# Kernel tuning notes

Hardware: AMD Instinct MI355X
Metric: run time of the kernel (lower is better)

Reference implementation:

```python
import jax, jax.numpy as jnp
import numpy as np

N, E = 20000, 320000
IN, HID, R, HEADS = 128, 256, 4, 4
C = HID // HEADS  # per-head dim


def setup_inputs() -> dict:
    key = jax.random.key(0)
    ks = jax.random.split(key, 20)
    g = lambda k, s, sc=0.05: jax.random.normal(k, s, jnp.float32) * sc
    return {
        'x': g(ks[0], (N, IN), 1.0),
        'edge_index': jax.random.randint(ks[1], (2, E), 0, N),
        'edge_type': jax.random.randint(ks[2], (E,), 0, R),
        'h_prev': g(ks[3], (N, HID), 1.0),
        # RGCN layer 1: relation weights, root weight, bias
        'W1': g(ks[4], (R, IN, HID)), 'root1': g(ks[5], (IN, HID)), 'b1': jnp.zeros((HID,), jnp.float32),
        # RGCN layer 2
        'W2': g(ks[6], (R, HID, HID)), 'root2': g(ks[7], (HID, HID)), 'b2': jnp.zeros((HID,), jnp.float32),
        # TransformerConv linears (query/key/value/skip), each Linear(HID, HEADS*C)
        'Wq': g(ks[8], (HID, HID)), 'bq': jnp.zeros((HID,), jnp.float32),
        'Wk': g(ks[9], (HID, HID)), 'bk': jnp.zeros((HID,), jnp.float32),
        'Wv': g(ks[10], (HID, HID)), 'bv': jnp.zeros((HID,), jnp.float32),
        'Wskip': g(ks[11], (HID, HID)), 'bskip': jnp.zeros((HID,), jnp.float32),
        # GRUCell (torch layout: [3*HID, in], gates ordered r, z, n)
        'W_ih': g(ks[12], (3 * HID, HID)), 'b_ih': jnp.zeros((3 * HID,), jnp.float32),
        'W_hh': g(ks[13], (3 * HID, HID)), 'b_hh': jnp.zeros((3 * HID,), jnp.float32),
    }


def rgcn(x, src, dst, etype, W, Wroot, b):
    # PyG RGCNConv: out_i = x_i @ Wroot + b + sum_r mean_{j in N_r(i)} x_j @ W_r
    n = x.shape[0]
    out = x @ Wroot + b
    xs = x[src]  # [E, F_in]
    for r in range(W.shape[0]):  # small fixed relation count
        mask = (etype == r).astype(x.dtype)  # [E]
        msg = (xs @ W[r]) * mask[:, None]  # [E, F_out]
        agg = jax.ops.segment_sum(msg, dst, num_segments=n)
        cnt = jax.ops.segment_sum(mask, dst, num_segments=n)
        out = out + agg / jnp.maximum(cnt, 1.0)[:, None]
    return out


def transformer_conv(x, src, dst, Wq, bq, Wk, bk, Wv, bv, Wskip, bskip):
    # PyG TransformerConv, concat=True, root_weight=True
    n = x.shape[0]
    q = (x @ Wq + bq).reshape(n, HEADS, C)
    k = (x @ Wk + bk).reshape(n, HEADS, C)
    v = (x @ Wv + bv).reshape(n, HEADS, C)
    score = jnp.einsum('ehc,ehc->eh', q[dst], k[src]) * (1.0 / np.sqrt(C))  # [E, H]
    smax = jax.ops.segment_max(score, dst, num_segments=n)  # [N, H]
    ex = jnp.exp(score - smax[dst])
    denom = jax.ops.segment_sum(ex, dst, num_segments=n)
    alpha = ex / jnp.maximum(denom[dst], 1e-16)  # edge softmax per dst node
    out = jax.ops.segment_sum(alpha[:, :, None] * v[src], dst, num_segments=n)  # [N, H, C]
    return out.reshape(n, HEADS * C) + x @ Wskip + bskip


def gru_cell(xi, h, W_ih, b_ih, W_hh, b_hh):
    gi = xi @ W_ih.T + b_ih
    gh = h @ W_hh.T + b_hh
    ir, iz, inn = jnp.split(gi, 3, axis=1)
    hr, hz, hn = jnp.split(gh, 3, axis=1)
    r = jax.nn.sigmoid(ir + hr)
    z = jax.nn.sigmoid(iz + hz)
    nw = jnp.tanh(inn + r * hn)
    return (1.0 - z) * nw + z * h


def reference(x, edge_index, edge_type, h_prev, W1, root1, b1, W2, root2, b2,
              Wq, bq, Wk, bk, Wv, bv, Wskip, bskip, W_ih, b_ih, W_hh, b_hh):
    src, dst = edge_index[0], edge_index[1]
    h = jax.nn.relu(rgcn(x, src, dst, edge_type, W1, root1, b1))
    h = jax.nn.relu(rgcn(h, src, dst, edge_type, W2, root2, b2))
    h = transformer_conv(h, src, dst, Wq, bq, Wk, bk, Wv, bv, Wskip, bskip)
    h = gru_cell(h, h_prev, W_ih, b_ih, W_hh, b_hh)
    return h
```

## Files before the change

kernel.cpp:

```cpp
#include <hip/hip_runtime.h>
#include <hip/hip_bf16.h>
#include <stdint.h>

#define N_NODES 20000
#define E_EDGES 320000
#define IN_F    128
#define HIDF    256
#define R_REL   4
#define NRKEYS  (N_NODES*R_REL)
#define SCAN_BLOCKS 80

typedef __attribute__((ext_vector_type(8))) short  short8;
typedef __attribute__((ext_vector_type(4))) float  floatx4;

__device__ __forceinline__ float bf2f(__hip_bfloat16 v){ return __bfloat162float(v); }
__device__ __forceinline__ __hip_bfloat16 f2bf(float v){ return __float2bfloat16(v); }
__device__ __forceinline__ float bfbits2f(unsigned short u){ return __uint_as_float(((unsigned)u)<<16); }
__device__ __forceinline__ unsigned short f2bfbits(float v){
    __hip_bfloat16 h = __float2bfloat16(v);
    return *(unsigned short*)&h;
}
__device__ __forceinline__ unsigned pack_bf2(float a, float b){
    return (unsigned)f2bfbits(a) | ((unsigned)f2bfbits(b) << 16);
}

__device__ __forceinline__ void gload_lds16(const void* g, void* l)
{
    __builtin_amdgcn_global_load_lds((const __attribute__((address_space(1))) void*)g,
                                     (__attribute__((address_space(3))) void*)l, 16, 0, 0);
}

template<int N>
__device__ __forceinline__ void wait_vm()
{
    if constexpr (N == 0)      asm volatile("s_waitcnt vmcnt(0)" ::: "memory");
    else if constexpr (N == 3) asm volatile("s_waitcnt vmcnt(3)" ::: "memory");
    else if constexpr (N == 4) asm volatile("s_waitcnt vmcnt(4)" ::: "memory");
    else if constexpr (N == 5) asm volatile("s_waitcnt vmcnt(5)" ::: "memory");
    else if constexpr (N == 8) asm volatile("s_waitcnt vmcnt(8)" ::: "memory");
    else                       asm volatile("s_waitcnt vmcnt(0)" ::: "memory");
}

__device__ __forceinline__ int2 xcd_swizzle()
{
    int gx = gridDim.x, gy = gridDim.y;
    int nwg = gx * gy;
    int lin = blockIdx.x + gx * blockIdx.y;
    int q = nwg >> 3, r = nwg & 7;
    int k = lin & 7, i = lin >> 3;
    int j = (k < r ? k*(q+1) : r*(q+1) + (k-r)*q) + i;
    return make_int2(j / gy, j % gy);
}

__global__ void count_kernel(const int* __restrict__ ei, const int* __restrict__ et,
                             int* __restrict__ cnt)
{
    int e = blockIdx.x*256 + threadIdx.x;
    if (e >= E_EDGES) return;
    int dst = ei[E_EDGES + e];
    atomicAdd(&cnt[dst*R_REL + et[e]], 1);
}

__global__ __launch_bounds__(1024) void scan_reduce_kernel(const int* __restrict__ cnt,
                                                           int* __restrict__ blocksum)
{
    int ix = blockIdx.x*1024 + threadIdx.x;
    int v = (ix < NRKEYS) ? cnt[ix] : 0;
    #pragma unroll
    for (int o=32;o>0;o>>=1) v += __shfl_xor(v, o, 64);
    __shared__ int wsum[16];
    int wave = threadIdx.x >> 6, lane = threadIdx.x & 63;
    if (lane == 0) wsum[wave] = v;
    __syncthreads();
    if (threadIdx.x == 0) {
        int s = 0;
        #pragma unroll
        for (int w=0;w<16;w++) s += wsum[w];
        blocksum[blockIdx.x] = s;
    }
}

__global__ __launch_bounds__(128) void scan_sums_kernel(const int* __restrict__ blocksum,
                                                        int* __restrict__ blockoff)
{
    __shared__ int s[128];
    int t = threadIdx.x;
    int v = (t < SCAN_BLOCKS) ? blocksum[t] : 0;
    s[t] = v; __syncthreads();
    for (int off=1; off<128; off<<=1) {
        int u = (t>=off) ? s[t-off] : 0;
        __syncthreads();
        s[t] += u;
        __syncthreads();
    }
    if (t < SCAN_BLOCKS) blockoff[t] = s[t] - v;
}

__global__ __launch_bounds__(1024) void scan_apply_kernel(const int* __restrict__ cnt,
                                                          const int* __restrict__ blockoff,
                                                          int* __restrict__ row_ptr,
                                                          int* __restrict__ cursor)
{
    __shared__ int s[1024];
    int t = threadIdx.x;
    int ix = blockIdx.x*1024 + t;
    int v = (ix < NRKEYS) ? cnt[ix] : 0;
    s[t] = v; __syncthreads();
    for (int off=1; off<1024; off<<=1) {
        int u = (t>=off) ? s[t-off] : 0;
        __syncthreads();
        s[t] += u;
        __syncthreads();
    }
    if (ix < NRKEYS) {
        int excl = blockoff[blockIdx.x] + s[t] - v;
        row_ptr[ix] = excl;
        cursor[ix]  = excl;
        if (ix == NRKEYS-1) row_ptr[NRKEYS] = excl + v;
    }
}

__global__ void fill_kernel(const int* __restrict__ ei, const int* __restrict__ et,
                            int* __restrict__ cursor, int* __restrict__ csr_src)
{
    int e = blockIdx.x*256 + threadIdx.x;
    if (e >= E_EDGES) return;
    int src = ei[e];
    int dst = ei[E_EDGES + e];
    int key = dst*R_REL + et[e];
    int pos = atomicAdd(&cursor[key], 1);
    csr_src[pos] = src;
}

__global__ void make_b1t(const float* __restrict__ root1,
                         const float* __restrict__ W1,
                         __hip_bfloat16* __restrict__ B1t)
{
    int idx = blockIdx.x*256 + threadIdx.x;
    if (idx >= 256*640) return;
    int n = idx / 640, k = idx % 640;
    float v;
    if (k < 128) v = root1[k*256 + n];
    else         v = W1[(k-128)*256 + n];
    B1t[idx] = f2bf(v);
}

__global__ void make_b2t(const float* __restrict__ root2,
                         const float* __restrict__ W2,
                         __hip_bfloat16* __restrict__ B2t)
{
    int idx = blockIdx.x*256 + threadIdx.x;
    if (idx >= 256*1280) return;
    int n = idx / 1280, k = idx % 1280;
    float v;
    if (k < 256) v = root2[k*256 + n];
    else         v = W2[(k-256)*256 + n];
    B2t[idx] = f2bf(v);
}

__global__ void make_b3t(const float* __restrict__ Wq, const float* __restrict__ Wk,
                         const float* __restrict__ Wv, const float* __restrict__ Wsk,
                         const float* __restrict__ bq, const float* __restrict__ bk,
                         const float* __restrict__ bv, const float* __restrict__ bsk,
                         __hip_bfloat16* __restrict__ B3t, float* __restrict__ bias3)
{
    int idx = blockIdx.x*256 + threadIdx.x;
    if (idx >= 1024*256) return;
    int n = idx / 256, k = idx % 256;
    int g = n >> 8, nn = n & 255;
    const float* W = (g==0)?Wq:(g==1)?Wk:(g==2)?Wv:Wsk;
    B3t[idx] = f2bf(W[k*256 + nn]);
    if (k == 0) {
        const float* B = (g==0)?bq:(g==1)?bk:(g==2)?bv:bsk;
        bias3[n] = B[nn];
    }
}

__global__ void cvt_f32_bf16(const float* __restrict__ in, __hip_bfloat16* __restrict__ out, int n)
{
    int i = blockIdx.x*256 + threadIdx.x;
    if (i < n) out[i] = f2bf(in[i]);
}

__global__ __launch_bounds__(256) void agg1_kernel(const float* __restrict__ x,
                                                   const int* __restrict__ row_ptr,
                                                   const int* __restrict__ csr_src,
                                                   __hip_bfloat16* __restrict__ A1)
{
    int b = blockIdx.x*4 + (threadIdx.x >> 6);
    int lane = threadIdx.x & 63;
    int i = b >> 2, r = b & 3;
    int e0 = row_ptr[b], e1 = row_ptr[b+1];
    float sx0=0.f,sy0=0.f, sx1=0.f,sy1=0.f, sx2=0.f,sy2=0.f, sx3=0.f,sy3=0.f;
    int e = e0;
    for (; e+4 <= e1; e += 4) {
        int i0=csr_src[e], i1=csr_src[e+1], i2=csr_src[e+2], i3=csr_src[e+3];
        float2 v0 = *(const float2*)(x + (size_t)i0*IN_F + lane*2);
        float2 v1 = *(const float2*)(x + (size_t)i1*IN_F + lane*2);
        float2 v2 = *(const float2*)(x + (size_t)i2*IN_F + lane*2);
        float2 v3 = *(const float2*)(x + (size_t)i3*IN_F + lane*2);
        sx0+=v0.x; sy0+=v0.y; sx1+=v1.x; sy1+=v1.y;
        sx2+=v2.x; sy2+=v2.y; sx3+=v3.x; sy3+=v3.y;
    }
    for (; e < e1; e++) {
        int i0 = csr_src[e];
        float2 v = *(const float2*)(x + (size_t)i0*IN_F + lane*2);
        sx0+=v.x; sy0+=v.y;
    }
    float sx = (sx0+sx1)+(sx2+sx3);
    float sy = (sy0+sy1)+(sy2+sy3);
    float inv = (e1>e0) ? 1.f/(float)(e1-e0) : 0.f;
    *(unsigned*)(A1 + (size_t)i*640 + 128 + r*128 + lane*2) = pack_bf2(sx*inv, sy*inv);
    if (r == 0) {
        float2 v = *(const float2*)(x + (size_t)i*IN_F + lane*2);
        *(unsigned*)(A1 + (size_t)i*640 + lane*2) = pack_bf2(v.x, v.y);
    }
}

__global__ __launch_bounds__(256) void agg2_kernel(const int* __restrict__ row_ptr,
                                                   const int* __restrict__ csr_src,
                                                   __hip_bfloat16* __restrict__ A2)
{
    int b = blockIdx.x*4 + (threadIdx.x >> 6);
    int lane = threadIdx.x & 63;
    int i = b >> 2, r = b & 3;
    int e0 = row_ptr[b], e1 = row_ptr[b+1];
    float a0=0.f,a1=0.f,a2=0.f,a3=0.f;
    float b0=0.f,b1=0.f,b2=0.f,b3=0.f;
    float c0=0.f,c1=0.f,c2=0.f,c3=0.f;
    float d0=0.f,d1=0.f,d2=0.f,d3=0.f;
    int e = e0;
    for (; e+4 <= e1; e += 4) {
        int i0=csr_src[e], i1=csr_src[e+1], i2=csr_src[e+2], i3=csr_src[e+3];
        ushort4 u0 = *(const ushort4*)(A2 + (size_t)i0*1280 + lane*4);
        ushort4 u1 = *(const ushort4*)(A2 + (size_t)i1*1280 + lane*4);
        ushort4 u2 = *(const ushort4*)(A2 + (size_t)i2*1280 + lane*4);
        ushort4 u3 = *(const ushort4*)(A2 + (size_t)i3*1280 + lane*4);
        a0+=bfbits2f(u0.x); a1+=bfbits2f(u0.y); a2+=bfbits2f(u0.z); a3+=bfbits2f(u0.w);
        b0+=bfbits2f(u1.x); b1+=bfbits2f(u1.y); b2+=bfbits2f(u1.z); b3+=bfbits2f(u1.w);
        c0+=bfbits2f(u2.x); c1+=bfbits2f(u2.y); c2+=bfbits2f(u2.z); c3+=bfbits2f(u2.w);
        d0+=bfbits2f(u3.x); d1+=bfbits2f(u3.y); d2+=bfbits2f(u3.z); d3+=bfbits2f(u3.w);
    }
    for (; e < e1; e++) {
        int i0 = csr_src[e];
        ushort4 u = *(const ushort4*)(A2 + (size_t)i0*1280 + lane*4);
        a0+=bfbits2f(u.x); a1+=bfbits2f(u.y); a2+=bfbits2f(u.z); a3+=bfbits2f(u.w);
    }
    float s0=(a0+b0)+(c0+d0), s1=(a1+b1)+(c1+d1), s2=(a2+b2)+(c2+d2), s3=(a3+b3)+(c3+d3);
    float inv = (e1>e0) ? 1.f/(float)(e1-e0) : 0.f;
    uint2 w;
    w.x = pack_bf2(s0*inv, s1*inv);
    w.y = pack_bf2(s2*inv, s3*inv);
    *(uint2*)(A2 + (size_t)i*1280 + 256 + r*256 + lane*4) = w;
}

template<int MI>
__device__ __forceinline__ void gemm_bt_body(const __hip_bfloat16* __restrict__ A, int lda,
                                             const __hip_bfloat16* __restrict__ Bt,
                                             const float* __restrict__ bias,
                                             __hip_bfloat16* __restrict__ C, int ldc,
                                             int M, int K, int relu,
                                             int tile_m, int tile_n,
                                             __hip_bfloat16* lds_a, __hip_bfloat16* lds_b)
{
    constexpr int A_ELEMS = MI*1024;
    constexpr int B_ELEMS = 4096;
    constexpr int L = MI/2 + 2;
    const int tid  = threadIdx.x;
    const int wave = tid >> 6;
    const int lane = tid & 63;
    const int wm = wave >> 1, wn = wave & 1;
    const int fm = lane & 15;
    const int q  = lane >> 4;
    const int sw = (q ^ ((fm >> 1) & 3)) * 8;

    floatx4 acc[MI][4];
    #pragma unroll
    for (int i=0;i<MI;i++)
        #pragma unroll
        for (int j=0;j<4;j++) acc[i][j] = (floatx4){0.f,0.f,0.f,0.f};

    const int srow   = lane >> 2;
    const int schunk = lane & 3;
    size_t a_goff[MI/2];
    #pragma unroll
    for (int s = 0; s < MI/2; ++s) {
        int r = (s*4 + wave)*16 + srow;
        int c = schunk ^ ((r >> 1) & 3);
        a_goff[s] = (size_t)min(tile_m + r, M-1)*lda + c*8;
    }
    size_t b_goff[2];
    #pragma unroll
    for (int s = 0; s < 2; ++s) {
        int r = (s*4 + wave)*16 + srow;
        int c = schunk ^ ((r >> 1) & 3);
        b_goff[s] = (size_t)(tile_n + r)*K + c*8;
    }

    const int nt = K >> 5;

    auto issue = [&](int t, int bufi) {
        const int kn = t << 5;
        #pragma unroll
        for (int s = 0; s < MI/2; ++s)
            gload_lds16(A + a_goff[s] + kn, lds_a + bufi*A_ELEMS + (s*4 + wave)*512);
        #pragma unroll
        for (int s = 0; s < 2; ++s)
            gload_lds16(Bt + b_goff[s] + kn, lds_b + bufi*B_ELEMS + (s*4 + wave)*512);
    };

    issue(0, 0);
    if (nt > 1) { issue(1, 1); wait_vm<L>(); }
    else        { wait_vm<0>(); }
    __builtin_amdgcn_s_barrier();

    int cur = 0, nx2 = 2;
    for (int t = 0; t < nt; ++t) {
        if (t + 2 < nt) issue(t + 2, nx2);

        const __hip_bfloat16* la = lds_a + cur*A_ELEMS;
        const __hip_bfloat16* lb = lds_b + cur*B_ELEMS;
        short8 afr[MI], bfr[4];
        #pragma unroll
        for (int i=0;i<MI;i++)
            afr[i] = *(const short8*)(la + (wm*(MI*16) + i*16 + fm)*32 + sw);
        #pragma unroll
        for (int j=0;j<4;j++)
            bfr[j] = *(const short8*)(lb + (wn*64 + j*16 + fm)*32 + sw);

        __builtin_amdgcn_s_setprio(1);
        #pragma unroll
        for (int i=0;i<MI;i++)
            #pragma unroll
            for (int j=0;j<4;j++)
                acc[i][j] = __builtin_amdgcn_mfma_f32_16x16x32_bf16(afr[i], bfr[j], acc[i][j], 0,0,0);
        __builtin_amdgcn_s_setprio(0);

        if (t + 1 < nt) {
            if (t + 2 < nt) wait_vm<L>();
            else            wait_vm<0>();
            __builtin_amdgcn_s_barrier();
            cur = (cur == 2) ? 0 : cur + 1;
            nx2 = (nx2 == 2) ? 0 : nx2 + 1;
        }
    }

    const int crow_base = tile_m + wm*(MI*16);
    const int ccol_base = tile_n + wn*64;
    #pragma unroll
    for (int i=0;i<MI;i++) {
        #pragma unroll
        for (int j=0;j<4;j++) {
            int c  = ccol_base + j*16 + fm;
            float bb = bias[c];
            #pragma unroll
            for (int rg=0; rg<4; rg++) {
                int r = crow_base + i*16 + q*4 + rg;
                if (r < M) {
                    float v = acc[i][j][rg] + bb;
                    if (relu) v = fmaxf(v, 0.f);
                    C[(size_t)r*ldc + c] = f2bf(v);
                }
            }
        }
    }
}

template<int MI>
__global__ __launch_bounds__(256) void gemm_bt_t(const __hip_bfloat16* __restrict__ A, int lda,
                                                 const __hip_bfloat16* __restrict__ Bt,
                                                 const float* __restrict__ bias,
                                                 __hip_bfloat16* __restrict__ C, int ldc,
                                                 int M, int K, int relu)
{
    __shared__ __align__(16) __hip_bfloat16 lds_a[3*MI*1024];
    __shared__ __align__(16) __hip_bfloat16 lds_b[3*4096];
    int2 xy = xcd_swizzle();
    gemm_bt_body<MI>(A, lda, Bt, bias, C, ldc, M, K, relu,
                     xy.x*(MI*32), xy.y*128, lds_a, lds_b);
}

__global__ __launch_bounds__(256) void gemm_gru_fused(
    const __hip_bfloat16* __restrict__ A0,
    const __hip_bfloat16* __restrict__ A1,
    const __hip_bfloat16* __restrict__ Bt0,
    const __hip_bfloat16* __restrict__ Bt1,
    const float* __restrict__ b_ih, const float* __restrict__ b_hh,
    const float* __restrict__ hprev, float* __restrict__ out)
{
    constexpr int BUF_ELEMS = 16384;
    __shared__ __align__(16) __hip_bfloat16 lds[2*BUF_ELEMS];
    int2 xy = xcd_swizzle();
    const int tile_m = xy.x * 64;
    const int c0     = xy.y * 64;
    const int tid = threadIdx.x, wave = tid >> 6, lane = tid & 63;
    const int wm = wave >> 1, wn = wave & 1;
    const int fm = lane & 15, q = lane >> 4;
    const int sw = (q ^ ((fm >> 1) & 3)) * 8;

    const int sub = lane >> 2, ch = lane & 3;
    const __hip_bfloat16* gsrc[8];
    int dstoff[8];
    #pragma unroll
    for (int s = 0; s < 8; ++s) {
        int seg = wave*8 + s;
        if (seg < 8) {
            int fr = seg*16 + sub;
            int mat = fr >> 6, rl = fr & 63;
            int c = ch ^ ((fr >> 1) & 3);
            int grow = min(tile_m + rl, N_NODES-1);
            gsrc[s] = (mat ? A1 : A0) + (size_t)grow*256 + c*8;
            dstoff[s] = seg*512;
        } else {
            int fs = seg - 8;
            int fr = fs*16 + sub;
            int grp = fr >> 6, ri = fr & 63;
            int mat = grp >= 3, gate = mat ? grp-3 : grp;
            int c = ch ^ ((fr >> 1) & 3);
            int grow = gate*256 + c0 + ri;
            gsrc[s] = (mat ? Bt1 : Bt0) + (size_t)grow*256 + c*8;
            dstoff[s] = 4096 + fs*512;
        }
    }

    floatx4 acc[2][3][2][2];
    #pragma unroll
    for (int m=0;m<2;m++)
        #pragma unroll
        for (int g=0;g<3;g++)
            #pragma unroll
            for (int i=0;i<2;i++)
                #pragma unroll
                for (int f=0;f<2;f++) acc[m][g][i][f] = (floatx4){0.f,0.f,0.f,0.f};

    auto issue = [&](int t, int bufi) {
        const int kn = t << 5;
        #pragma unroll
        for (int s = 0; s < 8; ++s)
            gload_lds16(gsrc[s] + kn, lds + bufi*BUF_ELEMS + dstoff[s]);
    };

    issue(0, 0);
    issue(1, 1);
    wait_vm<8>();
    __builtin_amdgcn_s_barrier();

    #pragma unroll 1
    for (int t = 0; t < 8; ++t) {
        const __hip_bfloat16* lb = lds + (t & 1)*BUF_ELEMS;
        short8 af[2][2], bfr[2][3][2];
        #pragma unroll
        for (int m=0;m<2;m++)
            #pragma unroll
            for (int i=0;i<2;i++)
                af[m][i] = *(const short8*)(lb + (m*64 + wm*32 + i*16 + fm)*32 + sw);
        #pragma unroll
        for (int m=0;m<2;m++)
            #pragma unroll
            for (int g=0;g<3;g++)
                #pragma unroll
                for (int f=0;f<2;f++)
                    bfr[m][g][f] = *(const short8*)(lb + 4096 + (((m*3+g)*64 + wn*32 + f*16 + fm)*32) + sw);

        __builtin_amdgcn_s_setprio(1);
        #pragma unroll
        for (int m=0;m<2;m++)
            #pragma unroll
            for (int g=0;g<3;g++)
                #pragma unroll
                for (int i=0;i<2;i++)
                    #pragma unroll
                    for (int f=0;f<2;f++)
                        acc[m][g][i][f] = __builtin_amdgcn_mfma_f32_16x16x32_bf16(af[m][i], bfr[m][g][f], acc[m][g][i][f], 0,0,0);
        __builtin_amdgcn_s_setprio(0);

        if (t + 1 < 8) {
            __builtin_amdgcn_s_barrier();
            if (t + 2 < 8) { issue(t + 2, t & 1); wait_vm<8>(); }
            else           wait_vm<0>();
            __builtin_amdgcn_s_barrier();
        }
    }

    #pragma unroll
    for (int f=0; f<2; ++f) {
        int c = c0 + wn*32 + f*16 + fm;
        float bir = b_ih[c], biz = b_ih[256+c], bin = b_ih[512+c];
        float bhr = b_hh[c], bhz = b_hh[256+c], bhn = b_hh[512+c];
        #pragma unroll
        for (int i=0; i<2; ++i) {
            #pragma unroll
            for (int rg=0; rg<4; ++rg) {
                int r = tile_m + wm*32 + i*16 + q*4 + rg;
                if (r < N_NODES) {
                    float gir = acc[0][0][i][f][rg] + bir;
                    float giz = acc[0][1][i][f][rg] + biz;
                    float gin = acc[0][2][i][f][rg] + bin;
                    float ghr = acc[1][0][i][f][rg] + bhr;
                    float ghz = acc[1][1][i][f][rg] + bhz;
                    float ghn = acc[1][2][i][f][rg] + bhn;
                    float rr = 1.f/(1.f + __expf(-(gir + ghr)));
                    float zz = 1.f/(1.f + __expf(-(giz + ghz)));
                    float xn = gin + rr*ghn;
                    float e2 = __expf(xn + xn);
                    float nn = 1.f - 2.f/(e2 + 1.f);
                    float h  = hprev[(size_t)r*256 + c];
                    out[(size_t)r*256 + c] = (1.f - zz)*nn + zz*h;
                }
            }
        }
    }
}

__global__ __launch_bounds__(256) void score_kernel(const __hip_bfloat16* __restrict__ qkvs,
                                                    const int* __restrict__ row_ptr,
                                                    const int* __restrict__ csr_src,
                                                    float* __restrict__ score)
{
    int i = blockIdx.x*4 + (threadIdx.x >> 6);
    int lane = threadIdx.x & 63;
    int h = lane >> 4, d4 = lane & 15;
    int e0 = row_ptr[i*R_REL], e1 = row_ptr[i*R_REL + R_REL];
    ushort4 qv = *(const ushort4*)(qkvs + (size_t)i*1024 + lane*4);
    float qx=bfbits2f(qv.x), qy=bfbits2f(qv.y), qz=bfbits2f(qv.z), qw=bfbits2f(qv.w);
    float* sp = score + (size_t)h*E_EDGES;
    int j = e0;
    for (; j+2 <= e1; j += 2) {
        int s0 = csr_src[j], s1 = csr_src[j+1];
        ushort4 k0 = *(const ushort4*)(qkvs + (size_t)s0*1024 + 256 + lane*4);
        ushort4 k1 = *(const ushort4*)(qkvs + (size_t)s1*1024 + 256 + lane*4);
        float d0 = qx*bfbits2f(k0.x)+qy*bfbits2f(k0.y)+qz*bfbits2f(k0.z)+qw*bfbits2f(k0.w);
        float d1 = qx*bfbits2f(k1.x)+qy*bfbits2f(k1.y)+qz*bfbits2f(k1.z)+qw*bfbits2f(k1.w);
        #pragma unroll
        for (int o=1;o<16;o<<=1){ d0 += __shfl_xor(d0,o,64); d1 += __shfl_xor(d1,o,64); }
        if (d4 == 0) { sp[j] = d0*0.125f; sp[j+1] = d1*0.125f; }
    }
    for (; j < e1; j++) {
        int s0 = csr_src[j];
        ushort4 k0 = *(const ushort4*)(qkvs + (size_t)s0*1024 + 256 + lane*4);
        float d0 = qx*bfbits2f(k0.x)+qy*bfbits2f(k0.y)+qz*bfbits2f(k0.z)+qw*bfbits2f(k0.w);
        #pragma unroll
        for (int o=1;o<16;o<<=1) d0 += __shfl_xor(d0,o,64);
        if (d4 == 0) sp[j] = d0*0.125f;
    }
}

__global__ __launch_bounds__(256) void attn_agg_kernel(const __hip_bfloat16* __restrict__ qkvs,
                                                       const float* __restrict__ score,
                                                       const int* __restrict__ row_ptr,
                                                       const int* __restrict__ csr_src,
                                                       __hip_bfloat16* __restrict__ hatt)
{
    int i = blockIdx.x*4 + (threadIdx.x >> 6);
    int lane = threadIdx.x & 63;
    int h  = lane >> 4;
    int d4 = lane & 15;
    int e0 = row_ptr[i*R_REL], e1 = row_ptr[i*R_REL + R_REL];
    int deg = e1 - e0;
    const float* sp = score + (size_t)h*E_EDGES + e0;

    float m = -1e30f;
    for (int j = d4; j < deg; j += 16) m = fmaxf(m, sp[j]);
    #pragma unroll
    for (int o=1;o<16;o<<=1) m = fmaxf(m, __shfl_xor(m, o, 64));

    float ssum = 0.f;
    for (int j = d4; j < deg; j += 16) ssum += __expf(sp[j] - m);
    #pragma unroll
    for (int o=1;o<16;o<<=1) ssum += __shfl_xor(ssum, o, 64);
    float inv = 1.f / fmaxf(ssum, 1e-16f);

    float ax=0.f, ay=0.f, az=0.f, aw=0.f;
    int j = 0;
    for (; j+4 <= deg; j += 4) {
        int s0=csr_src[e0+j], s1=csr_src[e0+j+1], s2=csr_src[e0+j+2], s3=csr_src[e0+j+3];
        float w0 = __expf(sp[j]   - m) * inv;
        float w1 = __expf(sp[j+1] - m) * inv;
        float w2 = __expf(sp[j+2] - m) * inv;
        float w3 = __expf(sp[j+3] - m) * inv;
        ushort4 u0 = *(const ushort4*)(qkvs + (size_t)s0*1024 + 512 + lane*4);
        ushort4 u1 = *(const ushort4*)(qkvs + (size_t)s1*1024 + 512 + lane*4);
        ushort4 u2 = *(const ushort4*)(qkvs + (size_t)s2*1024 + 512 + lane*4);
        ushort4 u3 = *(const ushort4*)(qkvs + (size_t)s3*1024 + 512 + lane*4);
        ax += w0*bfbits2f(u0.x) + w1*bfbits2f(u1.x) + w2*bfbits2f(u2.x) + w3*bfbits2f(u3.x);
        ay += w0*bfbits2f(u0.y) + w1*bfbits2f(u1.y) + w2*bfbits2f(u2.y) + w3*bfbits2f(u3.y);
        az += w0*bfbits2f(u0.z) + w1*bfbits2f(u1.z) + w2*bfbits2f(u2.z) + w3*bfbits2f(u3.z);
        aw += w0*bfbits2f(u0.w) + w1*bfbits2f(u1.w) + w2*bfbits2f(u2.w) + w3*bfbits2f(u3.w);
    }
    for (; j < deg; j++) {
        int s = csr_src[e0+j];
        float w = __expf(sp[j] - m) * inv;
        ushort4 u = *(const ushort4*)(qkvs + (size_t)s*1024 + 512 + lane*4);
        ax += w*bfbits2f(u.x); ay += w*bfbits2f(u.y);
        az += w*bfbits2f(u.z); aw += w*bfbits2f(u.w);
    }
    ushort4 sk = *(const ushort4*)(qkvs + (size_t)i*1024 + 768 + lane*4);
    uint2 w;
    w.x = pack_bf2(ax + bfbits2f(sk.x), ay + bfbits2f(sk.y));
    w.y = pack_bf2(az + bfbits2f(sk.z), aw + bfbits2f(sk.w));
    *(uint2*)(hatt + (size_t)i*256 + lane*4) = w;
}

extern "C" void kernel_launch(void* const* d_in, const int* in_sizes, int n_in,
                              void* d_out, int out_size, void* d_ws, size_t ws_size,
                              hipStream_t stream)
{
    const float* x       = (const float*)d_in[0];
    const int* edge_index= (const int*)d_in[1];
    const int* edge_type = (const int*)d_in[2];
    const float* hprev   = (const float*)d_in[3];
    const float* W1      = (const float*)d_in[4];
    const float* root1   = (const float*)d_in[5];
    const float* b1      = (const float*)d_in[6];
    const float* W2      = (const float*)d_in[7];
    const float* root2   = (const float*)d_in[8];
    const float* b2      = (const float*)d_in[9];
    const float* Wq      = (const float*)d_in[10];
    const float* bq      = (const float*)d_in[11];
    const float* Wk      = (const float*)d_in[12];
    const float* bk      = (const float*)d_in[13];
    const float* Wv      = (const float*)d_in[14];
    const float* bv      = (const float*)d_in[15];
    const float* Wskip   = (const float*)d_in[16];
    const float* bskip   = (const float*)d_in[17];
    const float* W_ih    = (const float*)d_in[18];
    const float* b_ih    = (const float*)d_in[19];
    const float* W_hh    = (const float*)d_in[20];
    const float* b_hh    = (const float*)d_in[21];

    char* ws = (char*)d_ws;
    size_t off = 0;
    auto take = [&](size_t bytes)->char* {
        char* p = ws + off;
        off = (off + bytes + 255) & ~(size_t)255;
        return p;
    };
    int* cnt        = (int*)take((size_t)NRKEYS*4);
    int* row_ptr    = (int*)take((size_t)(NRKEYS+1)*4);
    int* cursor     = (int*)take((size_t)NRKEYS*4);
    int* csr_src    = (int*)take((size_t)E_EDGES*4);
    int* blocksum   = (int*)take((size_t)SCAN_BLOCKS*4);
    int* blockoff   = (int*)take((size_t)(SCAN_BLOCKS+1)*4);
    float* score    = (float*)take((size_t)R_REL*E_EDGES*4);
    __hip_bfloat16* B1t   = (__hip_bfloat16*)take((size_t)256*640*2);
    __hip_bfloat16* B2t   = (__hip_bfloat16*)take((size_t)256*1280*2);
    __hip_bfloat16* B3t   = (__hip_bfloat16*)take((size_t)1024*256*2);
    __hip_bfloat16* Biht  = (__hip_bfloat16*)take((size_t)768*256*2);
    __hip_bfloat16* Bhht  = (__hip_bfloat16*)take((size_t)768*256*2);
    float*          bias3 = (float*)take((size_t)1024*4);
    __hip_bfloat16* hprev_bf = (__hip_bfloat16*)take((size_t)N_NODES*256*2);
    char* P1 = take((size_t)N_NODES*640*2);
    char* P2 = take((size_t)N_NODES*1536*2);

    __hip_bfloat16* A1   = (__hip_bfloat16*)P1;
    __hip_bfloat16* h2   = (__hip_bfloat16*)P1;
    __hip_bfloat16* hatt = (__hip_bfloat16*)P1;
    __hip_bfloat16* A2   = (__hip_bfloat16*)P2;
    __hip_bfloat16* qkvs = (__hip_bfloat16*)P2;

    hipMemsetAsync(cnt, 0, (size_t)NRKEYS*4, stream);
    count_kernel<<<(E_EDGES+255)/256, 256, 0, stream>>>(edge_index, edge_type, cnt);
    scan_reduce_kernel<<<SCAN_BLOCKS, 1024, 0, stream>>>(cnt, blocksum);
    scan_sums_kernel<<<1, 128, 0, stream>>>(blocksum, blockoff);
    scan_apply_kernel<<<SCAN_BLOCKS, 1024, 0, stream>>>(cnt, blockoff, row_ptr, cursor);
    fill_kernel<<<(E_EDGES+255)/256, 256, 0, stream>>>(edge_index, edge_type, cursor, csr_src);

    make_b1t<<<(256*640+255)/256, 256, 0, stream>>>(root1, W1, B1t);
    make_b2t<<<(256*1280+255)/256, 256, 0, stream>>>(root2, W2, B2t);
    make_b3t<<<(1024*256+255)/256, 256, 0, stream>>>(Wq, Wk, Wv, Wskip, bq, bk, bv, bskip, B3t, bias3);
    cvt_f32_bf16<<<(768*256+255)/256, 256, 0, stream>>>(W_ih, Biht, 768*256);
    cvt_f32_bf16<<<(768*256+255)/256, 256, 0, stream>>>(W_hh, Bhht, 768*256);
    cvt_f32_bf16<<<(N_NODES*256+255)/256, 256, 0, stream>>>(hprev, hprev_bf, N_NODES*256);

    agg1_kernel<<<NRKEYS/4, 256, 0, stream>>>(x, row_ptr, csr_src, A1);

    dim3 g12(313, 2);
    gemm_bt_t<2><<<g12, 256, 0, stream>>>(A1, 640, B1t, b1, A2, 1280, N_NODES, 640, 1);

    agg2_kernel<<<NRKEYS/4, 256, 0, stream>>>(row_ptr, csr_src, A2);

    gemm_bt_t<2><<<g12, 256, 0, stream>>>(A2, 1280, B2t, b2, h2, 256, N_NODES, 1280, 1);

    dim3 g3(157, 8);
    gemm_bt_t<4><<<g3, 256, 0, stream>>>(h2, 256, B3t, bias3, qkvs, 1024, N_NODES, 256, 0);

    score_kernel<<<N_NODES/4, 256, 0, stream>>>(qkvs, row_ptr, csr_src, score);
    attn_agg_kernel<<<N_NODES/4, 256, 0, stream>>>(qkvs, score, row_ptr, csr_src, hatt);

    gemm_gru_fused<<<dim3(313, 4), 256, 0, stream>>>(hatt, hprev_bf, Biht, Bhht,
                                                     b_ih, b_hh, hprev, (float*)d_out);
}
```

Before: 426.4 us.

## Split neighbor gathers across half-waves, gather bf16 x, and enlarge GRU GEMM tile

The layer-1 aggregation now reads a bf16 copy of x, produced by an extra conversion kernel, instead of fp32 rows. Both aggregation kernels split each wave into two half-waves that process alternate edges with wider per-lane loads, then combine the halves with a cross-lane shuffle. This is meant to cut gather bytes and raise memory-level parallelism. The fused GRU GEMM moves to 512-thread blocks covering 128 rows, with matching LDS layout and load segmentation, so each B-weight tile is reused across more rows. The costs are an extra conversion pass over x, slight rounding of x before summation, and possibly lower occupancy in the larger GRU blocks.

```diff
diff --git a/kernel.cpp b/kernel.cpp
--- a/kernel.cpp
+++ b/kernel.cpp
@@ -182,7 +182,7 @@
     if (i < n) out[i] = f2bf(in[i]);
 }
 
-__global__ __launch_bounds__(256) void agg1_kernel(const float* __restrict__ x,
+__global__ __launch_bounds__(256) void agg1_kernel(const __hip_bfloat16* __restrict__ xbf,
                                                    const int* __restrict__ row_ptr,
                                                    const int* __restrict__ csr_src,
                                                    __hip_bfloat16* __restrict__ A1)
@@ -190,30 +190,30 @@
     int b = blockIdx.x*4 + (threadIdx.x >> 6);
     int lane = threadIdx.x & 63;
     int i = b >> 2, r = b & 3;
+    int half = lane >> 5, l32 = lane & 31;
     int e0 = row_ptr[b], e1 = row_ptr[b+1];
-    float sx0=0.f,sy0=0.f, sx1=0.f,sy1=0.f, sx2=0.f,sy2=0.f, sx3=0.f,sy3=0.f;
-    int e = e0;
-    for (; e+4 <= e1; e += 4) {
-        int i0=csr_src[e], i1=csr_src[e+1], i2=csr_src[e+2], i3=csr_src[e+3];
-        float2 v0 = *(const float2*)(x + (size_t)i0*IN_F + lane*2);
-        float2 v1 = *(const float2*)(x + (size_t)i1*IN_F + lane*2);
-        float2 v2 = *(const float2*)(x + (size_t)i2*IN_F + lane*2);
-        float2 v3 = *(const float2*)(x + (size_t)i3*IN_F + lane*2);
-        sx0+=v0.x; sy0+=v0.y; sx1+=v1.x; sy1+=v1.y;
-        sx2+=v2.x; sy2+=v2.y; sx3+=v3.x; sy3+=v3.y;
-    }
-    for (; e < e1; e++) {
-        int i0 = csr_src[e];
-        float2 v = *(const float2*)(x + (size_t)i0*IN_F + lane*2);
-        sx0+=v.x; sy0+=v.y;
-    }
-    float sx = (sx0+sx1)+(sx2+sx3);
-    float sy = (sy0+sy1)+(sy2+sy3);
+    float s0=0.f, s1=0.f, s2=0.f, s3=0.f;
+    for (int j = e0; j < e1; j += 2) {
+        int je = j + half;
+        if (je < e1) {
+            int src = csr_src[je];
+            ushort4 u = *(const ushort4*)(xbf + (size_t)src*IN_F + l32*4);
+            s0 += bfbits2f(u.x); s1 += bfbits2f(u.y);
+            s2 += bfbits2f(u.z); s3 += bfbits2f(u.w);
+        }
+    }
+    s0 += __shfl_xor(s0, 32, 64);
+    s1 += __shfl_xor(s1, 32, 64);
+    s2 += __shfl_xor(s2, 32, 64);
+    s3 += __shfl_xor(s3, 32, 64);
     float inv = (e1>e0) ? 1.f/(float)(e1-e0) : 0.f;
-    *(unsigned*)(A1 + (size_t)i*640 + 128 + r*128 + lane*2) = pack_bf2(sx*inv, sy*inv);
-    if (r == 0) {
-        float2 v = *(const float2*)(x + (size_t)i*IN_F + lane*2);
-        *(unsigned*)(A1 + (size_t)i*640 + lane*2) = pack_bf2(v.x, v.y);
+    if (half == 0) {
+        uint2 w;
+        w.x = pack_bf2(s0*inv, s1*inv);
+        w.y = pack_bf2(s2*inv, s3*inv);
+        *(uint2*)(A1 + (size_t)i*640 + 128 + r*128 + l32*4) = w;
+        if (r == 0)
+            *(uint2*)(A1 + (size_t)i*640 + l32*4) = *(const uint2*)(xbf + (size_t)i*IN_F + l32*4);
     }
 }
 
@@ -224,34 +224,31 @@
     int b = blockIdx.x*4 + (threadIdx.x >> 6);
     int lane = threadIdx.x & 63;
     int i = b >> 2, r = b & 3;
+    int half = lane >> 5, l32 = lane & 31;
     int e0 = row_ptr[b], e1 = row_ptr[b+1];
-    float a0=0.f,a1=0.f,a2=0.f,a3=0.f;
-    float b0=0.f,b1=0.f,b2=0.f,b3=0.f;
-    float c0=0.f,c1=0.f,c2=0.f,c3=0.f;
-    float d0=0.f,d1=0.f,d2=0.f,d3=0.f;
-    int e = e0;
-    for (; e+4 <= e1; e += 4) {
-        int i0=csr_src[e], i1=csr_src[e+1], i2=csr_src[e+2], i3=csr_src[e+3];
-        ushort4 u0 = *(const ushort4*)(A2 + (size_t)i0*1280 + lane*4);
-        ushort4 u1 = *(const ushort4*)(A2 + (size_t)i1*1280 + lane*4);
-        ushort4 u2 = *(const ushort4*)(A2 + (size_t)i2*1280 + lane*4);
-        ushort4 u3 = *(const ushort4*)(A2 + (size_t)i3*1280 + lane*4);
-        a0+=bfbits2f(u0.x); a1+=bfbits2f(u0.y); a2+=bfbits2f(u0.z); a3+=bfbits2f(u0.w);
-        b0+=bfbits2f(u1.x); b1+=bfbits2f(u1.y); b2+=bfbits2f(u1.z); b3+=bfbits2f(u1.w);
-        c0+=bfbits2f(u2.x); c1+=bfbits2f(u2.y); c2+=bfbits2f(u2.z); c3+=bfbits2f(u2.w);
-        d0+=bfbits2f(u3.x); d1+=bfbits2f(u3.y); d2+=bfbits2f(u3.z); d3+=bfbits2f(u3.w);
-    }
-    for (; e < e1; e++) {
-        int i0 = csr_src[e];
-        ushort4 u = *(const ushort4*)(A2 + (size_t)i0*1280 + lane*4);
-        a0+=bfbits2f(u.x); a1+=bfbits2f(u.y); a2+=bfbits2f(u.z); a3+=bfbits2f(u.w);
-    }
-    float s0=(a0+b0)+(c0+d0), s1=(a1+b1)+(c1+d1), s2=(a2+b2)+(c2+d2), s3=(a3+b3)+(c3+d3);
+    float a[8];
+    #pragma unroll
+    for (int k=0;k<8;k++) a[k] = 0.f;
+    for (int j = e0; j < e1; j += 2) {
+        int je = j + half;
+        if (je < e1) {
+            int src = csr_src[je];
+            short8 u = *(const short8*)(A2 + (size_t)src*1280 + l32*8);
+            #pragma unroll
+            for (int k=0;k<8;k++) a[k] += bfbits2f((unsigned short)u[k]);
+        }
+    }
+    #pragma unroll
+    for (int k=0;k<8;k++) a[k] += __shfl_xor(a[k], 32, 64);
     float inv = (e1>e0) ? 1.f/(float)(e1-e0) : 0.f;
-    uint2 w;
-    w.x = pack_bf2(s0*inv, s1*inv);
-    w.y = pack_bf2(s2*inv, s3*inv);
-    *(uint2*)(A2 + (size_t)i*1280 + 256 + r*256 + lane*4) = w;
+    if (half == 0) {
+        uint4 w;
+        w.x = pack_bf2(a[0]*inv, a[1]*inv);
+        w.y = pack_bf2(a[2]*inv, a[3]*inv);
+        w.z = pack_bf2(a[4]*inv, a[5]*inv);
+        w.w = pack_bf2(a[6]*inv, a[7]*inv);
+        *(uint4*)(A2 + (size_t)i*1280 + 256 + r*256 + l32*8) = w;
+    }
 }
 
 template<int MI>
@@ -380,7 +377,7 @@
                      xy.x*(MI*32), xy.y*128, lds_a, lds_b);
 }
 
-__global__ __launch_bounds__(256) void gemm_gru_fused(
+__global__ __launch_bounds__(512) void gemm_gru_fused(
     const __hip_bfloat16* __restrict__ A0,
     const __hip_bfloat16* __restrict__ A1,
     const __hip_bfloat16* __restrict__ Bt0,
@@ -388,10 +385,10 @@
     const float* __restrict__ b_ih, const float* __restrict__ b_hh,
     const float* __restrict__ hprev, float* __restrict__ out)
 {
-    constexpr int BUF_ELEMS = 16384;
+    constexpr int BUF_ELEMS = 20480;
     __shared__ __align__(16) __hip_bfloat16 lds[2*BUF_ELEMS];
     int2 xy = xcd_swizzle();
-    const int tile_m = xy.x * 64;
+    const int tile_m = xy.x * 128;
     const int c0     = xy.y * 64;
     const int tid = threadIdx.x, wave = tid >> 6, lane = tid & 63;
     const int wm = wave >> 1, wn = wave & 1;
@@ -399,27 +396,27 @@
     const int sw = (q ^ ((fm >> 1) & 3)) * 8;
 
     const int sub = lane >> 2, ch = lane & 3;
-    const __hip_bfloat16* gsrc[8];
-    int dstoff[8];
-    #pragma unroll
-    for (int s = 0; s < 8; ++s) {
-        int seg = wave*8 + s;
-        if (seg < 8) {
+    const __hip_bfloat16* gsrc[5];
+    int dstoff[5];
+    #pragma unroll
+    for (int s = 0; s < 5; ++s) {
+        int seg = wave*5 + s;
+        if (seg < 16) {
             int fr = seg*16 + sub;
-            int mat = fr >> 6, rl = fr & 63;
+            int mat = fr >> 7, rl = fr & 127;
             int c = ch ^ ((fr >> 1) & 3);
             int grow = min(tile_m + rl, N_NODES-1);
             gsrc[s] = (mat ? A1 : A0) + (size_t)grow*256 + c*8;
             dstoff[s] = seg*512;
         } else {
-            int fs = seg - 8;
+            int fs = seg - 16;
             int fr = fs*16 + sub;
             int grp = fr >> 6, ri = fr & 63;
             int mat = grp >= 3, gate = mat ? grp-3 : grp;
             int c = ch ^ ((fr >> 1) & 3);
             int grow = gate*256 + c0 + ri;
             gsrc[s] = (mat ? Bt1 : Bt0) + (size_t)grow*256 + c*8;
-            dstoff[s] = 4096 + fs*512;
+            dstoff[s] = 8192 + fs*512;
         }
     }
 
@@ -436,13 +433,13 @@
     auto issue = [&](int t, int bufi) {
         const int kn = t << 5;
         #pragma unroll
-        for (int s = 0; s < 8; ++s)
+        for (int s = 0; s < 5; ++s)
             gload_lds16(gsrc[s] + kn, lds + bufi*BUF_ELEMS + dstoff[s]);
     };
 
     issue(0, 0);
     issue(1, 1);
-    wait_vm<8>();
+    wait_vm<5>();
     __builtin_amdgcn_s_barrier();
 
     #pragma unroll 1
@@ -453,14 +450,14 @@
         for (int m=0;m<2;m++)
             #pragma unroll
             for (int i=0;i<2;i++)
-                af[m][i] = *(const short8*)(lb + (m*64 + wm*32 + i*16 + fm)*32 + sw);
+                af[m][i] = *(const short8*)(lb + (m*128 + wm*32 + i*16 + fm)*32 + sw);
         #pragma unroll
         for (int m=0;m<2;m++)
             #pragma unroll
             for (int g=0;g<3;g++)
                 #pragma unroll
                 for (int f=0;f<2;f++)
-                    bfr[m][g][f] = *(const short8*)(lb + 4096 + (((m*3+g)*64 + wn*32 + f*16 + fm)*32) + sw);
+                    bfr[m][g][f] = *(const short8*)(lb + 8192 + (((m*3+g)*64 + wn*32 + f*16 + fm)*32) + sw);
 
         __builtin_amdgcn_s_setprio(1);
         #pragma unroll
@@ -476,7 +473,7 @@
 
         if (t + 1 < 8) {
             __builtin_amdgcn_s_barrier();
-            if (t + 2 < 8) { issue(t + 2, t & 1); wait_vm<8>(); }
+            if (t + 2 < 8) { issue(t + 2, t & 1); wait_vm<5>(); }
             else           wait_vm<0>();
             __builtin_amdgcn_s_barrier();
         }
@@ -649,6 +646,7 @@
     __hip_bfloat16* Bhht  = (__hip_bfloat16*)take((size_t)768*256*2);
     float*          bias3 = (float*)take((size_t)1024*4);
     __hip_bfloat16* hprev_bf = (__hip_bfloat16*)take((size_t)N_NODES*256*2);
+    __hip_bfloat16* xbf      = (__hip_bfloat16*)take((size_t)N_NODES*IN_F*2);
     char* P1 = take((size_t)N_NODES*640*2);
     char* P2 = take((size_t)N_NODES*1536*2);
 
@@ -671,8 +669,9 @@
     cvt_f32_bf16<<<(768*256+255)/256, 256, 0, stream>>>(W_ih, Biht, 768*256);
     cvt_f32_bf16<<<(768*256+255)/256, 256, 0, stream>>>(W_hh, Bhht, 768*256);
     cvt_f32_bf16<<<(N_NODES*256+255)/256, 256, 0, stream>>>(hprev, hprev_bf, N_NODES*256);
-
-    agg1_kernel<<<NRKEYS/4, 256, 0, stream>>>(x, row_ptr, csr_src, A1);
+    cvt_f32_bf16<<<(N_NODES*IN_F+255)/256, 256, 0, stream>>>(x, xbf, N_NODES*IN_F);
+
+    agg1_kernel<<<NRKEYS/4, 256, 0, stream>>>(xbf, row_ptr, csr_src, A1);
 
     dim3 g12(313, 2);
     gemm_bt_t<2><<<g12, 256, 0, stream>>>(A1, 640, B1t, b1, A2, 1280, N_NODES, 640, 1);
@@ -687,6 +686,6 @@
     score_kernel<<<N_NODES/4, 256, 0, stream>>>(qkvs, row_ptr, csr_src, score);
     attn_agg_kernel<<<N_NODES/4, 256, 0, stream>>>(qkvs, score, row_ptr, csr_src, hatt);
 
-    gemm_gru_fused<<<dim3(313, 4), 256, 0, stream>>>(hatt, hprev_bf, Biht, Bhht,
+    gemm_gru_fused<<<dim3(157, 4), 512, 0, stream>>>(hatt, hprev_bf, Biht, Bhht,
                                                      b_ih, b_hh, hprev, (float*)d_out);
 }
```

Result: no change. 434.1 us (+1.8%).
